# Optimization experiments

Hardware: AMD Instinct MI355X
Metric: run time of the kernel (lower is better)

Reference implementation:

```python
import jax, jax.numpy as jnp
import numpy as np

F = 128      # n_features
H = 512      # size_hidden
NT = 1       # n_targets
B = 512      # batch
T = 512      # seq_len


def setup_inputs() -> dict:
    key = jax.random.key(0)
    ks = jax.random.split(key, 7)
    s_ih = 1.0 / np.sqrt(H)
    return {
        "X": jax.random.normal(ks[0], (B, T, F), dtype=jnp.float32),
        # LSTMCell params (torch layout: [4H, in], gate order i, f, g, o)
        "W_ih": jax.random.uniform(ks[1], (4 * H, F), jnp.float32, -s_ih, s_ih),
        "W_hh": jax.random.uniform(ks[2], (4 * H, H), jnp.float32, -s_ih, s_ih),
        "b_ih": jax.random.uniform(ks[3], (4 * H,), jnp.float32, -s_ih, s_ih),
        "b_hh": jax.random.uniform(ks[4], (4 * H,), jnp.float32, -s_ih, s_ih),
        # final linear: size_hidden -> n_targets
        "W_out": jax.random.uniform(ks[5], (NT, H), jnp.float32, -s_ih, s_ih),
        "b_out": jax.random.uniform(ks[6], (NT,), jnp.float32, -s_ih, s_ih),
    }


def reference(X, W_ih, W_hh, b_ih, b_hh, W_out, b_out):
    Bsz = X.shape[0]
    Hd = W_hh.shape[1]

    # precompute input-to-gate projection for all timesteps: [B, T, 4H]
    x_gates = jnp.einsum('btf,gf->btg', X, W_ih) + b_ih + b_hh

    def step(carry, xg_t):
        h, c = carry
        gates = xg_t + h @ W_hh.T                      # [B, 4H]
        i, f, g, o = jnp.split(gates, 4, axis=-1)
        i = jax.nn.sigmoid(i)
        f = jax.nn.sigmoid(f)
        g = jnp.tanh(g)
        o = jax.nn.sigmoid(o)
        c = f * c + i * g
        h = o * jnp.tanh(c)
        out_t = h @ W_out.T + b_out                    # [B, NT]
        return (h, c), out_t

    h0 = jnp.zeros((Bsz, Hd), dtype=X.dtype)
    c0 = jnp.zeros((Bsz, Hd), dtype=X.dtype)
    xg = jnp.swapaxes(x_gates, 0, 1)                   # [T, B, 4H]
    _, outs = jax.lax.scan(step, (h0, c0), xg)         # [T, B, NT]
    return jnp.swapaxes(outs, 0, 1)                    # [B, T, NT]
```

## Files before the change

### kernel.cpp

```cpp
#include <hip/hip_runtime.h>

#define Hd   512
#define Fd   128
#define Td   512
#define Bd   512
#define TG   64
#define BG   64
#define WPG  32
#define LDW  648
#define LDH  520
#define LDG  68

typedef __bf16 bf16x8 __attribute__((ext_vector_type(8)));
typedef float  f32x4  __attribute__((ext_vector_type(4)));
typedef unsigned int u32x4 __attribute__((ext_vector_type(4)));
typedef unsigned int u32x2 __attribute__((ext_vector_type(2)));

__device__ __forceinline__ unsigned short f2bf(float x) {
    unsigned u = __float_as_uint(x);
    unsigned r = (u + 0x7fffu + ((u >> 16) & 1u)) >> 16;
    return (unsigned short)r;
}
__device__ __forceinline__ float sigm(float x) {
    return 1.0f / (1.0f + __expf(-x));
}
__device__ __forceinline__ float tanh_fast(float x) {
    float xc = fminf(fmaxf(x, -15.f), 15.f);
    float e  = __expf(2.f * xc);
    return (e - 1.f) / (e + 1.f);
}

__global__ __launch_bounds__(256, 1) void lstm_persist(
    const float* __restrict__ X,     const float* __restrict__ W_ih,
    const float* __restrict__ W_hh,  const float* __restrict__ b_ih,
    const float* __restrict__ b_hh,  const float* __restrict__ W_out,
    const float* __restrict__ b_out, float* __restrict__ out,
    unsigned short* __restrict__ hbuf,
    unsigned int*  __restrict__ bar)
{
    extern __shared__ char smem[];
    unsigned short* Wl    = (unsigned short*)smem;
    unsigned short* htile = (unsigned short*)(smem + TG * LDW * 2);
    float*          gsum  = (float*)(smem + TG * LDW * 2);
    float*          biasl = (float*)(smem + TG * LDW * 2 + TG * LDH * 2);
    float*          hpart = biasl + TG;

    const int tid = threadIdx.x;
    const int gid = blockIdx.x;
    const int grp = gid & 7;
    const int r   = gid >> 3;
    const int bb  = grp * BG;
    const int jb  = r * 16;

    for (int i = tid; i < TG * (Hd / 4); i += 256) {
        int lr = i >> 7, q = (i & 127) << 2;
        int grow = ((lr >> 4) * Hd) + jb + (lr & 15);
        float4 w = *(const float4*)(W_hh + (size_t)grow * Hd + q);
        ushort4 p; p.x = f2bf(w.x); p.y = f2bf(w.y); p.z = f2bf(w.z); p.w = f2bf(w.w);
        *(ushort4*)(Wl + lr * LDW + q) = p;
    }
    for (int i = tid; i < TG * (Fd / 4); i += 256) {
        int lr = i >> 5, q = (i & 31) << 2;
        int grow = ((lr >> 4) * Hd) + jb + (lr & 15);
        float4 w = *(const float4*)(W_ih + (size_t)grow * Fd + q);
        ushort4 p; p.x = f2bf(w.x); p.y = f2bf(w.y); p.z = f2bf(w.z); p.w = f2bf(w.w);
        *(ushort4*)(Wl + lr * LDW + 512 + q) = p;
    }
    if (tid < TG) {
        int grow = ((tid >> 4) * Hd) + jb + (tid & 15);
        biasl[tid] = b_ih[grow] + b_hh[grow];
    }
    __syncthreads();

    const int lane = tid & 63, wid = tid >> 6;
    const int m16  = lane & 15, quad = lane >> 4;
    const int gr0  = (wid & 1) * 32;
    const int bt0  = (wid >> 1) * 32;
    const unsigned short* wl0 = Wl + (gr0 + m16) * LDW + quad * 8;
    const unsigned short* wl1 = wl0 + 16 * LDW;
    const int brow0 = bb + bt0 + m16;
    const int brow1 = brow0 + 16;
    const unsigned short* hl0 = htile + (bt0 + m16) * LDH + quad * 8;
    const unsigned short* hl1 = hl0 + 16 * LDH;

    const int eb  = tid & 63;
    const int jjb = (tid >> 6) << 2;
    float wout[4];
#pragma unroll
    for (int u = 0; u < 4; ++u) wout[u] = W_out[jb + jjb + u];
    const float bo = b_out[0];
    float cst[4] = {0.f, 0.f, 0.f, 0.f};

    unsigned int* mybar = bar + grp * 32;
    unsigned short* hw_lds = htile + (size_t)(tid >> 6) * LDH + (tid & 63) * 8;

    f32x4 acc00, acc01, acc10, acc11;
    const float* xp0 = X + (size_t)brow0 * (Td * Fd) + quad * 8;
    const float* xp1 = X + (size_t)brow1 * (Td * Fd) + quad * 8;

    auto do_xpart = [&]() {
#pragma unroll
        for (int ks = 0; ks < 4; ++ks) {
            bf16x8 a0 = *(const bf16x8*)(wl0 + 512 + ks * 32);
            bf16x8 a1 = *(const bf16x8*)(wl1 + 512 + ks * 32);
            float4 xa = *(const float4*)(xp0 + ks * 32);
            float4 xb = *(const float4*)(xp0 + ks * 32 + 4);
            float4 ya = *(const float4*)(xp1 + ks * 32);
            float4 yb = *(const float4*)(xp1 + ks * 32 + 4);
            bf16x8 b0, b1;
            b0[0]=(__bf16)xa.x; b0[1]=(__bf16)xa.y; b0[2]=(__bf16)xa.z; b0[3]=(__bf16)xa.w;
            b0[4]=(__bf16)xb.x; b0[5]=(__bf16)xb.y; b0[6]=(__bf16)xb.z; b0[7]=(__bf16)xb.w;
            b1[0]=(__bf16)ya.x; b1[1]=(__bf16)ya.y; b1[2]=(__bf16)ya.z; b1[3]=(__bf16)ya.w;
            b1[4]=(__bf16)yb.x; b1[5]=(__bf16)yb.y; b1[6]=(__bf16)yb.z; b1[7]=(__bf16)yb.w;
            acc00 = __builtin_amdgcn_mfma_f32_16x16x32_bf16(a0, b0, acc00, 0, 0, 0);
            acc01 = __builtin_amdgcn_mfma_f32_16x16x32_bf16(a0, b1, acc01, 0, 0, 0);
            acc10 = __builtin_amdgcn_mfma_f32_16x16x32_bf16(a1, b0, acc10, 0, 0, 0);
            acc11 = __builtin_amdgcn_mfma_f32_16x16x32_bf16(a1, b1, acc11, 0, 0, 0);
        }
    };

    acc00 = f32x4{0.f,0.f,0.f,0.f}; acc01 = f32x4{0.f,0.f,0.f,0.f};
    acc10 = f32x4{0.f,0.f,0.f,0.f}; acc11 = f32x4{0.f,0.f,0.f,0.f};
    do_xpart();

    for (int t = 0; t < Td; ++t) {
        if (t > 0 && tid == 0) {
            unsigned tgt = (unsigned)t * WPG;
            while (__hip_atomic_load(mybar, __ATOMIC_RELAXED, __HIP_MEMORY_SCOPE_AGENT) < tgt)
                __builtin_amdgcn_s_sleep(2);
        }
        __syncthreads();

        const unsigned short* hprev = hbuf + (size_t)((t & 1) ^ 1) * (Bd * Hd);

        u32x4 hv0,hv1,hv2,hv3,hv4,hv5,hv6,hv7,hv8,hv9,hv10,hv11,hv12,hv13,hv14,hv15;
        {
            const unsigned short* p0 =
                hprev + (size_t)(bb + (tid >> 6)) * Hd + (tid & 63) * 8;
            const unsigned short* b0p = p0 + 1 * 2048;
            const unsigned short* b1p = p0 + 3 * 2048;
            const unsigned short* b2p = p0 + 5 * 2048;
            const unsigned short* b3p = p0 + 7 * 2048;
            const unsigned short* b4p = p0 + 9 * 2048;
            const unsigned short* b5p = p0 + 11 * 2048;
            const unsigned short* b6p = p0 + 13 * 2048;
            const unsigned short* b7p = p0 + 15 * 2048;
            asm volatile(
                "global_load_dwordx4 %0,  %16, off offset:-4096 sc1\n\t"
                "global_load_dwordx4 %1,  %16, off sc1\n\t"
                "global_load_dwordx4 %2,  %17, off offset:-4096 sc1\n\t"
                "global_load_dwordx4 %3,  %17, off sc1\n\t"
                "global_load_dwordx4 %4,  %18, off offset:-4096 sc1\n\t"
                "global_load_dwordx4 %5,  %18, off sc1\n\t"
                "global_load_dwordx4 %6,  %19, off offset:-4096 sc1\n\t"
                "global_load_dwordx4 %7,  %19, off sc1\n\t"
                "global_load_dwordx4 %8,  %20, off offset:-4096 sc1\n\t"
                "global_load_dwordx4 %9,  %20, off sc1\n\t"
                "global_load_dwordx4 %10, %21, off offset:-4096 sc1\n\t"
                "global_load_dwordx4 %11, %21, off sc1\n\t"
                "global_load_dwordx4 %12, %22, off offset:-4096 sc1\n\t"
                "global_load_dwordx4 %13, %22, off sc1\n\t"
                "global_load_dwordx4 %14, %23, off offset:-4096 sc1\n\t"
                "global_load_dwordx4 %15, %23, off sc1\n\t"
                "s_waitcnt vmcnt(0)"
                : "=&v"(hv0), "=&v"(hv1), "=&v"(hv2), "=&v"(hv3),
                  "=&v"(hv4), "=&v"(hv5), "=&v"(hv6), "=&v"(hv7),
                  "=&v"(hv8), "=&v"(hv9), "=&v"(hv10), "=&v"(hv11),
                  "=&v"(hv12), "=&v"(hv13), "=&v"(hv14), "=&v"(hv15)
                : "v"(b0p), "v"(b1p), "v"(b2p), "v"(b3p),
                  "v"(b4p), "v"(b5p), "v"(b6p), "v"(b7p)
                : "memory");
        }
        *(u32x4*)(hw_lds + 0 * 2080)  = hv0;  *(u32x4*)(hw_lds + 1 * 2080)  = hv1;
        *(u32x4*)(hw_lds + 2 * 2080)  = hv2;  *(u32x4*)(hw_lds + 3 * 2080)  = hv3;
        *(u32x4*)(hw_lds + 4 * 2080)  = hv4;  *(u32x4*)(hw_lds + 5 * 2080)  = hv5;
        *(u32x4*)(hw_lds + 6 * 2080)  = hv6;  *(u32x4*)(hw_lds + 7 * 2080)  = hv7;
        *(u32x4*)(hw_lds + 8 * 2080)  = hv8;  *(u32x4*)(hw_lds + 9 * 2080)  = hv9;
        *(u32x4*)(hw_lds + 10 * 2080) = hv10; *(u32x4*)(hw_lds + 11 * 2080) = hv11;
        *(u32x4*)(hw_lds + 12 * 2080) = hv12; *(u32x4*)(hw_lds + 13 * 2080) = hv13;
        *(u32x4*)(hw_lds + 14 * 2080) = hv14; *(u32x4*)(hw_lds + 15 * 2080) = hv15;
        __syncthreads();

#pragma unroll 4
        for (int ks = 0; ks < 16; ++ks) {
            bf16x8 a0 = *(const bf16x8*)(wl0 + ks * 32);
            bf16x8 a1 = *(const bf16x8*)(wl1 + ks * 32);
            bf16x8 b0 = *(const bf16x8*)(hl0 + ks * 32);
            bf16x8 b1 = *(const bf16x8*)(hl1 + ks * 32);
            acc00 = __builtin_amdgcn_mfma_f32_16x16x32_bf16(a0, b0, acc00, 0, 0, 0);
            acc01 = __builtin_amdgcn_mfma_f32_16x16x32_bf16(a0, b1, acc01, 0, 0, 0);
            acc10 = __builtin_amdgcn_mfma_f32_16x16x32_bf16(a1, b0, acc10, 0, 0, 0);
            acc11 = __builtin_amdgcn_mfma_f32_16x16x32_bf16(a1, b1, acc11, 0, 0, 0);
        }
        __syncthreads();

        {
            const int row = gr0 + (quad << 2);
            const int col = bt0 + m16;
            float* g00 = gsum + row * LDG + col;
            float* g10 = gsum + (row + 16) * LDG + col;
#pragma unroll
            for (int v = 0; v < 4; ++v) {
                g00[v * LDG]      = acc00[v];
                g00[v * LDG + 16] = acc01[v];
                g10[v * LDG]      = acc10[v];
                g10[v * LDG + 16] = acc11[v];
            }
        }
        __syncthreads();

        float part = 0.f;
        unsigned short hvb[4];
#pragma unroll
        for (int u = 0; u < 4; ++u) {
            int jj = jjb + u;
            float pi = gsum[jj * LDG + eb]        + biasl[jj];
            float pf = gsum[(16 + jj) * LDG + eb] + biasl[16 + jj];
            float pg = gsum[(32 + jj) * LDG + eb] + biasl[32 + jj];
            float po = gsum[(48 + jj) * LDG + eb] + biasl[48 + jj];
            float ii = sigm(pi), ff = sigm(pf);
            float gg = tanh_fast(pg), oo = sigm(po);
            float c  = ff * cst[u] + ii * gg;
            cst[u]   = c;
            float h  = oo * tanh_fast(c);
            hvb[u]   = f2bf(h);
            part    += h * wout[u];
        }
        {
            u32x2 hd2;
            hd2[0] = (unsigned)hvb[0] | ((unsigned)hvb[1] << 16);
            hd2[1] = (unsigned)hvb[2] | ((unsigned)hvb[3] << 16);
            unsigned short* hwp =
                hbuf + (size_t)(t & 1) * (Bd * Hd) + (size_t)(bb + eb) * Hd + jb + jjb;
            asm volatile("global_store_dwordx2 %0, %1, off sc1"
                         :: "v"(hwp), "v"(hd2) : "memory");
            asm volatile("s_waitcnt vmcnt(0)" ::: "memory");
        }
        if (tid == 0)
            __hip_atomic_fetch_add(mybar, 1u, __ATOMIC_RELAXED, __HIP_MEMORY_SCOPE_AGENT);

        hpart[tid] = part;

        acc00 = f32x4{0.f,0.f,0.f,0.f}; acc01 = f32x4{0.f,0.f,0.f,0.f};
        acc10 = f32x4{0.f,0.f,0.f,0.f}; acc11 = f32x4{0.f,0.f,0.f,0.f};
        if (t + 1 < Td) {
            xp0 += Fd; xp1 += Fd;
            do_xpart();
        }

        __syncthreads();
        if (tid < 64) {
            float s = hpart[tid] + hpart[tid + 64] + hpart[tid + 128] + hpart[tid + 192];
            if (r == 0) s += bo;
            atomicAdd(out + (size_t)(bb + tid) * Td + t, s);
        }
    }
}

extern "C" void kernel_launch(void* const* d_in, const int* in_sizes, int n_in,
                              void* d_out, int out_size, void* d_ws, size_t ws_size,
                              hipStream_t stream) {
    const float* X     = (const float*)d_in[0];
    const float* W_ih  = (const float*)d_in[1];
    const float* W_hh  = (const float*)d_in[2];
    const float* b_ih  = (const float*)d_in[3];
    const float* b_hh  = (const float*)d_in[4];
    const float* W_out = (const float*)d_in[5];
    const float* b_out = (const float*)d_in[6];
    float* out = (float*)d_out;

    unsigned short* hbuf = (unsigned short*)d_ws;
    unsigned int*   bar  = (unsigned int*)((char*)d_ws + 2u * Bd * Hd * 2u);

    hipMemsetAsync(d_ws, 0, 2u * Bd * Hd * 2u + 4096u, stream);
    hipMemsetAsync(d_out, 0, (size_t)out_size * sizeof(float), stream);

    const size_t smem = (size_t)TG * LDW * 2
                      + (size_t)TG * LDH * 2
                      + TG * 4 + 256 * 4;
    (void)hipFuncSetAttribute((const void*)lstm_persist,
                              hipFuncAttributeMaxDynamicSharedMemorySize, (int)smem);

    lstm_persist<<<dim3(256), dim3(256), smem, stream>>>(
        X, W_ih, W_hh, b_ih, b_hh, W_out, b_out, out, hbuf, bar);
}
```

Measured before the change: 3.686 ms.

## Replace counter barrier with per-block flags and compute output from staged h

The shared atomic counter barrier becomes per-block flag slots. Each block stores its own step number, and a whole wavefront polls all 32 flags with a ballot. The output projection no longer uses per-timestep global atomicAdds of partial sums. Each block now computes full dot products for two batch rows from the already-loaded previous h tile, delayed by one step through an extra loop iteration, and the d_out memset is removed. This cuts atomic contention and the serialized fetch-add, but adds an extra iteration and uses bf16-rounded h for the output.

```diff
diff --git a/kernel.cpp b/kernel.cpp
--- a/kernel.cpp
+++ b/kernel.cpp
@@ -20,6 +20,9 @@
     unsigned u = __float_as_uint(x);
     unsigned r = (u + 0x7fffu + ((u >> 16) & 1u)) >> 16;
     return (unsigned short)r;
+}
+__device__ __forceinline__ float bf2f(unsigned short b) {
+    return __uint_as_float((unsigned)b << 16);
 }
 __device__ __forceinline__ float sigm(float x) {
     return 1.0f / (1.0f + __expf(-x));
@@ -43,7 +46,7 @@
     unsigned short* htile = (unsigned short*)(smem + TG * LDW * 2);
     float*          gsum  = (float*)(smem + TG * LDW * 2);
     float*          biasl = (float*)(smem + TG * LDW * 2 + TG * LDH * 2);
-    float*          hpart = biasl + TG;
+    float*          osum  = biasl + TG;
 
     const int tid = threadIdx.x;
     const int gid = blockIdx.x;
@@ -85,11 +88,13 @@
 
     const int eb  = tid & 63;
     const int jjb = (tid >> 6) << 2;
-    float wout[4];
-#pragma unroll
-    for (int u = 0; u < 4; ++u) wout[u] = W_out[jb + jjb + u];
     const float bo = b_out[0];
     float cst[4] = {0.f, 0.f, 0.f, 0.f};
+
+    const int pb2 = tid >> 7;
+    const int hh4 = (tid & 127) << 2;
+    const float4 wo4 = *(const float4*)(W_out + hh4);
+    const unsigned short* hrow = htile + (2 * r + pb2) * LDH + hh4;
 
     unsigned int* mybar = bar + grp * 32;
     unsigned short* hw_lds = htile + (size_t)(tid >> 6) * LDH + (tid & 63) * 8;
@@ -123,11 +128,14 @@
     acc10 = f32x4{0.f,0.f,0.f,0.f}; acc11 = f32x4{0.f,0.f,0.f,0.f};
     do_xpart();
 
-    for (int t = 0; t < Td; ++t) {
-        if (t > 0 && tid == 0) {
-            unsigned tgt = (unsigned)t * WPG;
-            while (__hip_atomic_load(mybar, __ATOMIC_RELAXED, __HIP_MEMORY_SCOPE_AGENT) < tgt)
-                __builtin_amdgcn_s_sleep(2);
+    for (int t = 0; t <= Td; ++t) {
+        if (t > 0) {
+            const unsigned int* fp = mybar + (lane & 31);
+            for (;;) {
+                unsigned v = __hip_atomic_load(fp, __ATOMIC_RELAXED, __HIP_MEMORY_SCOPE_AGENT);
+                if (__ballot(v < (unsigned)t) == 0ull) break;
+                __builtin_amdgcn_s_sleep(1);
+            }
         }
         __syncthreads();
 
@@ -181,18 +189,36 @@
         *(u32x4*)(hw_lds + 14 * 2080) = hv14; *(u32x4*)(hw_lds + 15 * 2080) = hv15;
         __syncthreads();
 
+        if (t < Td) {
 #pragma unroll 4
-        for (int ks = 0; ks < 16; ++ks) {
-            bf16x8 a0 = *(const bf16x8*)(wl0 + ks * 32);
-            bf16x8 a1 = *(const bf16x8*)(wl1 + ks * 32);
-            bf16x8 b0 = *(const bf16x8*)(hl0 + ks * 32);
-            bf16x8 b1 = *(const bf16x8*)(hl1 + ks * 32);
-            acc00 = __builtin_amdgcn_mfma_f32_16x16x32_bf16(a0, b0, acc00, 0, 0, 0);
-            acc01 = __builtin_amdgcn_mfma_f32_16x16x32_bf16(a0, b1, acc01, 0, 0, 0);
-            acc10 = __builtin_amdgcn_mfma_f32_16x16x32_bf16(a1, b0, acc10, 0, 0, 0);
-            acc11 = __builtin_amdgcn_mfma_f32_16x16x32_bf16(a1, b1, acc11, 0, 0, 0);
-        }
-        __syncthreads();
+            for (int ks = 0; ks < 16; ++ks) {
+                bf16x8 a0 = *(const bf16x8*)(wl0 + ks * 32);
+                bf16x8 a1 = *(const bf16x8*)(wl1 + ks * 32);
+                bf16x8 b0 = *(const bf16x8*)(hl0 + ks * 32);
+                bf16x8 b1 = *(const bf16x8*)(hl1 + ks * 32);
+                acc00 = __builtin_amdgcn_mfma_f32_16x16x32_bf16(a0, b0, acc00, 0, 0, 0);
+                acc01 = __builtin_amdgcn_mfma_f32_16x16x32_bf16(a0, b1, acc01, 0, 0, 0);
+                acc10 = __builtin_amdgcn_mfma_f32_16x16x32_bf16(a1, b0, acc10, 0, 0, 0);
+                acc11 = __builtin_amdgcn_mfma_f32_16x16x32_bf16(a1, b1, acc11, 0, 0, 0);
+            }
+        }
+
+        if (t > 0) {
+            ushort4 hv = *(const ushort4*)hrow;
+            float s = bf2f(hv.x) * wo4.x + bf2f(hv.y) * wo4.y
+                    + bf2f(hv.z) * wo4.z + bf2f(hv.w) * wo4.w;
+#pragma unroll
+            for (int off = 32; off >= 1; off >>= 1) s += __shfl_down(s, off);
+            if (lane == 0) osum[wid] = s;
+        }
+        __syncthreads();
+
+        if (t > 0 && tid < 2) {
+            float o = osum[2 * tid] + osum[2 * tid + 1] + bo;
+            out[(size_t)(bb + 2 * r + tid) * Td + (t - 1)] = o;
+        }
+
+        if (t == Td) break;
 
         {
             const int row = gr0 + (quad << 2);
@@ -209,7 +235,6 @@
         }
         __syncthreads();
 
-        float part = 0.f;
         unsigned short hvb[4];
 #pragma unroll
         for (int u = 0; u < 4; ++u) {
@@ -224,7 +249,6 @@
             cst[u]   = c;
             float h  = oo * tanh_fast(c);
             hvb[u]   = f2bf(h);
-            part    += h * wout[u];
         }
         {
             u32x2 hd2;
@@ -236,23 +260,17 @@
                          :: "v"(hwp), "v"(hd2) : "memory");
             asm volatile("s_waitcnt vmcnt(0)" ::: "memory");
         }
+        __syncthreads();
+
         if (tid == 0)
-            __hip_atomic_fetch_add(mybar, 1u, __ATOMIC_RELAXED, __HIP_MEMORY_SCOPE_AGENT);
-
-        hpart[tid] = part;
+            __hip_atomic_store(mybar + r, (unsigned)(t + 1),
+                               __ATOMIC_RELAXED, __HIP_MEMORY_SCOPE_AGENT);
 
         acc00 = f32x4{0.f,0.f,0.f,0.f}; acc01 = f32x4{0.f,0.f,0.f,0.f};
         acc10 = f32x4{0.f,0.f,0.f,0.f}; acc11 = f32x4{0.f,0.f,0.f,0.f};
         if (t + 1 < Td) {
             xp0 += Fd; xp1 += Fd;
             do_xpart();
-        }
-
-        __syncthreads();
-        if (tid < 64) {
-            float s = hpart[tid] + hpart[tid + 64] + hpart[tid + 128] + hpart[tid + 192];
-            if (r == 0) s += bo;
-            atomicAdd(out + (size_t)(bb + tid) * Td + t, s);
         }
     }
 }
@@ -273,11 +291,10 @@
     unsigned int*   bar  = (unsigned int*)((char*)d_ws + 2u * Bd * Hd * 2u);
 
     hipMemsetAsync(d_ws, 0, 2u * Bd * Hd * 2u + 4096u, stream);
-    hipMemsetAsync(d_out, 0, (size_t)out_size * sizeof(float), stream);
 
     const size_t smem = (size_t)TG * LDW * 2
                       + (size_t)TG * LDH * 2
-                      + TG * 4 + 256 * 4;
+                      + TG * 4 + 64;
     (void)hipFuncSetAttribute((const void*)lstm_persist,
                               hipFuncAttributeMaxDynamicSharedMemorySize, (int)smem);
 
```

Result: slower. 3.851 ms (+4.5%).
